# Optimization experiments

Measured on AMD Instinct MI355X. Metric: run time of the kernel, lower is better.

## Reference

```python
import jax, jax.numpy as jnp
import numpy as np


def setup_inputs() -> dict:
    key = jax.random.key(0)
    ks = jax.random.split(key, 7)
    B, NU, NI, F, L = 16384, 100000, 100000, 512, 256
    x = jax.random.randint(ks[0], (B, 2), 0, min(NU, NI), dtype=jnp.int64)
    user_lookup = jax.random.normal(ks[1], (NU, F), dtype=jnp.float32)
    item_lookup = jax.random.normal(ks[2], (NI, F), dtype=jnp.float32)
    s = 1.0 / np.sqrt(F)
    user_W = jax.random.normal(ks[3], (L, F), dtype=jnp.float32) * s
    user_b = jax.random.normal(ks[4], (L,), dtype=jnp.float32) * s
    item_W = jax.random.normal(ks[5], (L, F), dtype=jnp.float32) * s
    item_b = jax.random.normal(ks[6], (L,), dtype=jnp.float32) * s
    return {"x": x, "user_lookup": user_lookup, "item_lookup": item_lookup,
            "user_W": user_W, "user_b": user_b, "item_W": item_W, "item_b": item_b}


def _encode(feats, W, b):
    # Linear (torch weight layout [out, in]) + relu, the mDA encoder
    return jax.nn.relu(jnp.einsum('bf,lf->bl', feats, W) + b)


def reference(x, user_lookup, item_lookup, user_W, user_b, item_W, item_b):
    user_x = user_lookup[x[:, 0]]            # [B, F] gather
    item_x = item_lookup[x[:, 1]]            # [B, F] gather
    user_latent = _encode(user_x, user_W, user_b)   # [B, L]
    item_latent = _encode(item_x, item_W, item_b)   # [B, L]
    # diag(U @ I.T) == rowwise dot; same math, no [B,B] intermediate
    diagonal = jnp.sum(user_latent * item_latent, axis=-1)
    return diagonal[:, None]                 # [B, 1]
```

## Files before the change

### kernel.cpp

```cpp
#include <hip/hip_runtime.h>
#include <stdint.h>

#define B_TOTAL 16384
#define F 512
#define L 256
#define TB 32
#define KC 64
#define LDP 72

typedef _Float16 half8 __attribute__((ext_vector_type(8)));
typedef float floatx4 __attribute__((ext_vector_type(4)));

__device__ __align__(16) _Float16 g_wt[2][8][L][KC];

__global__ void wconv_kernel(const float* __restrict__ uW,
                             const float* __restrict__ iW) {
    int tid = blockIdx.x * blockDim.x + threadIdx.x;
    int which = tid >> 17;
    int r = tid & 131071;
    int l = r >> 9;
    int f = r & 511;
    float v = which ? iW[r] : uW[r];
    g_wt[which][f >> 6][l][f & 63] = (_Float16)v;
}

__launch_bounds__(256, 3)
__global__ void fused_kernel(const int* __restrict__ x,
                             const float* __restrict__ ulook,
                             const float* __restrict__ ilook,
                             const float* __restrict__ ub,
                             const float* __restrict__ ib,
                             float* __restrict__ out) {
    __shared__ _Float16 sA[TB][LDP];
    __shared__ _Float16 sB[L][LDP];
    __shared__ float    sRed[TB];
    __shared__ int      sIdx[2][TB];

    const int t = threadIdx.x;
    const int bbase = blockIdx.x * TB;

    if (t < 2 * TB) {
        int r = t >> 1, c = t & 1;
        sIdx[c][r] = x[(bbase + r) * 2 + c];
    }
    if (t < TB) sRed[t] = 0.0f;
    __syncthreads();

    const int wave = t >> 6;
    const int lane = t & 63;
    const int l15  = lane & 15;
    const int quad = lane >> 4;
    const int nbase = wave * 64;

    floatx4 ulat[2][4];
    floatx4 acc[2][4];

    const int arow = t >> 3;
    const int aoff = (t & 7) * 8;

    #pragma unroll 1
    for (int pass = 0; pass < 2; ++pass) {
        const float* __restrict__ look = pass ? ilook : ulook;
        const float* __restrict__ bias = pass ? ib : ub;

        #pragma unroll
        for (int mt = 0; mt < 2; ++mt)
            #pragma unroll
            for (int nt = 0; nt < 4; ++nt) {
                floatx4 z = {0.f, 0.f, 0.f, 0.f};
                acc[mt][nt] = z;
            }

        const int rowidx = sIdx[pass][arow];
        const float* asrc_base = look + (size_t)rowidx * F + aoff;

        #pragma unroll 1
        for (int ks = 0; ks < 8; ++ks) {
            __syncthreads();

            {
                const float* src = asrc_base + ks * KC;
                float4 v0 = *(const float4*)(src);
                float4 v1 = *(const float4*)(src + 4);
                _Float16 h[8];
                h[0] = (_Float16)v0.x; h[1] = (_Float16)v0.y;
                h[2] = (_Float16)v0.z; h[3] = (_Float16)v0.w;
                h[4] = (_Float16)v1.x; h[5] = (_Float16)v1.y;
                h[6] = (_Float16)v1.z; h[7] = (_Float16)v1.w;
                *(half8*)(&sA[arow][aoff]) = *(half8*)h;
            }
            {
                const _Float16* src = &g_wt[pass][ks][0][0];
                #pragma unroll
                for (int i = 0; i < 8; ++i) {
                    int c = t + 256 * i;
                    int rowb = c >> 3;
                    int offb = (c & 7) * 8;
                    uint4 v = *(const uint4*)(src + c * 8);
                    *(uint4*)(&sB[rowb][offb]) = v;
                }
            }
            __syncthreads();

            #pragma unroll
            for (int kt = 0; kt < 2; ++kt) {
                half8 af[2], bfr[4];
                #pragma unroll
                for (int mt = 0; mt < 2; ++mt)
                    af[mt] = *(const half8*)(&sA[mt * 16 + l15][kt * 32 + quad * 8]);
                #pragma unroll
                for (int nt = 0; nt < 4; ++nt)
                    bfr[nt] = *(const half8*)(&sB[nbase + nt * 16 + l15][kt * 32 + quad * 8]);
                #pragma unroll
                for (int mt = 0; mt < 2; ++mt)
                    #pragma unroll
                    for (int nt = 0; nt < 4; ++nt)
                        acc[mt][nt] = __builtin_amdgcn_mfma_f32_16x16x32_f16(
                            af[mt], bfr[nt], acc[mt][nt], 0, 0, 0);
            }
        }

        if (pass == 0) {
            #pragma unroll
            for (int mt = 0; mt < 2; ++mt)
                #pragma unroll
                for (int nt = 0; nt < 4; ++nt) {
                    int n = nbase + nt * 16 + l15;
                    float bv = bias[n];
                    #pragma unroll
                    for (int r = 0; r < 4; ++r) {
                        float v = acc[mt][nt][r] + bv;
                        ulat[mt][nt][r] = v > 0.f ? v : 0.f;
                    }
                }
        } else {
            #pragma unroll
            for (int mt = 0; mt < 2; ++mt) {
                float partial[4] = {0.f, 0.f, 0.f, 0.f};
                #pragma unroll
                for (int nt = 0; nt < 4; ++nt) {
                    int n = nbase + nt * 16 + l15;
                    float bv = bias[n];
                    #pragma unroll
                    for (int r = 0; r < 4; ++r) {
                        float v = acc[mt][nt][r] + bv;
                        v = v > 0.f ? v : 0.f;
                        partial[r] += v * ulat[mt][nt][r];
                    }
                }
                #pragma unroll
                for (int r = 0; r < 4; ++r) {
                    float v = partial[r];
                    v += __shfl_xor(v, 1);
                    v += __shfl_xor(v, 2);
                    v += __shfl_xor(v, 4);
                    v += __shfl_xor(v, 8);
                    if (l15 == 0)
                        atomicAdd(&sRed[mt * 16 + quad * 4 + r], v);
                }
            }
        }
    }

    __syncthreads();
    if (t < TB) out[bbase + t] = sRed[t];
}

extern "C" void kernel_launch(void* const* d_in, const int* in_sizes, int n_in,
                              void* d_out, int out_size, void* d_ws, size_t ws_size,
                              hipStream_t stream) {
    const int*   x     = (const int*)d_in[0];
    const float* ulook = (const float*)d_in[1];
    const float* ilook = (const float*)d_in[2];
    const float* uW    = (const float*)d_in[3];
    const float* ub    = (const float*)d_in[4];
    const float* iW    = (const float*)d_in[5];
    const float* ib    = (const float*)d_in[6];
    float* out = (float*)d_out;

    wconv_kernel<<<1024, 256, 0, stream>>>(uW, iW);
    fused_kernel<<<B_TOTAL / TB, 256, 0, stream>>>(x, ulook, ilook, ub, ib, out);
}
```

Measured before the change: 346.1 us.

## Load weight fragments directly from global and prefetch gathered rows

The shared-memory staging of the fp16 weight tile is removed, and each wave now reads its MFMA B fragments straight from the global pre-converted weight buffer, relying on L2/L1 caching. The gathered embedding-row load for the next K-chunk is issued before the MFMA work of the current chunk to overlap latency. Launch bounds occupancy hint drops from 3 to 2 blocks per CU, and LDS use shrinks. The risk is that the direct global B reads, each wave fetching 64-row strided fragments, are less efficient than the coalesced LDS staging and add latency on the MFMA critical path.

```diff
diff --git a/kernel.cpp b/kernel.cpp
--- a/kernel.cpp
+++ b/kernel.cpp
@@ -18,13 +18,12 @@
     int tid = blockIdx.x * blockDim.x + threadIdx.x;
     int which = tid >> 17;
     int r = tid & 131071;
-    int l = r >> 9;
     int f = r & 511;
     float v = which ? iW[r] : uW[r];
-    g_wt[which][f >> 6][l][f & 63] = (_Float16)v;
+    g_wt[which][f >> 6][r >> 9][f & 63] = (_Float16)v;
 }
 
-__launch_bounds__(256, 3)
+__launch_bounds__(256, 2)
 __global__ void fused_kernel(const int* __restrict__ x,
                              const float* __restrict__ ulook,
                              const float* __restrict__ ilook,
@@ -32,7 +31,6 @@
                              const float* __restrict__ ib,
                              float* __restrict__ out) {
     __shared__ _Float16 sA[TB][LDP];
-    __shared__ _Float16 sB[L][LDP];
     __shared__ float    sRed[TB];
     __shared__ int      sIdx[2][TB];
 
@@ -72,52 +70,53 @@
             }
 
         const int rowidx = sIdx[pass][arow];
-        const float* asrc_base = look + (size_t)rowidx * F + aoff;
+        const float* asrc = look + (size_t)rowidx * F + aoff;
+
+        float4 p0 = *(const float4*)(asrc);
+        float4 p1 = *(const float4*)(asrc + 4);
 
         #pragma unroll 1
         for (int ks = 0; ks < 8; ++ks) {
             __syncthreads();
 
             {
-                const float* src = asrc_base + ks * KC;
-                float4 v0 = *(const float4*)(src);
-                float4 v1 = *(const float4*)(src + 4);
                 _Float16 h[8];
-                h[0] = (_Float16)v0.x; h[1] = (_Float16)v0.y;
-                h[2] = (_Float16)v0.z; h[3] = (_Float16)v0.w;
-                h[4] = (_Float16)v1.x; h[5] = (_Float16)v1.y;
-                h[6] = (_Float16)v1.z; h[7] = (_Float16)v1.w;
+                h[0] = (_Float16)p0.x; h[1] = (_Float16)p0.y;
+                h[2] = (_Float16)p0.z; h[3] = (_Float16)p0.w;
+                h[4] = (_Float16)p1.x; h[5] = (_Float16)p1.y;
+                h[6] = (_Float16)p1.z; h[7] = (_Float16)p1.w;
                 *(half8*)(&sA[arow][aoff]) = *(half8*)h;
             }
-            {
-                const _Float16* src = &g_wt[pass][ks][0][0];
-                #pragma unroll
-                for (int i = 0; i < 8; ++i) {
-                    int c = t + 256 * i;
-                    int rowb = c >> 3;
-                    int offb = (c & 7) * 8;
-                    uint4 v = *(const uint4*)(src + c * 8);
-                    *(uint4*)(&sB[rowb][offb]) = v;
-                }
+            if (ks < 7) {
+                const float* src = asrc + (ks + 1) * KC;
+                p0 = *(const float4*)(src);
+                p1 = *(const float4*)(src + 4);
             }
             __syncthreads();
 
+            const _Float16* __restrict__ bb = &g_wt[pass][ks][0][0];
+            half8 bfr[2][4];
             #pragma unroll
-            for (int kt = 0; kt < 2; ++kt) {
-                half8 af[2], bfr[4];
+            for (int kt = 0; kt < 2; ++kt)
+                #pragma unroll
+                for (int nt = 0; nt < 4; ++nt)
+                    bfr[kt][nt] = *(const half8*)(bb + (nbase + nt * 16 + l15) * KC
+                                                     + kt * 32 + quad * 8);
+            half8 af[2][2];
+            #pragma unroll
+            for (int kt = 0; kt < 2; ++kt)
                 #pragma unroll
                 for (int mt = 0; mt < 2; ++mt)
-                    af[mt] = *(const half8*)(&sA[mt * 16 + l15][kt * 32 + quad * 8]);
-                #pragma unroll
-                for (int nt = 0; nt < 4; ++nt)
-                    bfr[nt] = *(const half8*)(&sB[nbase + nt * 16 + l15][kt * 32 + quad * 8]);
+                    af[kt][mt] = *(const half8*)(&sA[mt * 16 + l15][kt * 32 + quad * 8]);
+
+            #pragma unroll
+            for (int kt = 0; kt < 2; ++kt)
                 #pragma unroll
                 for (int mt = 0; mt < 2; ++mt)
                     #pragma unroll
                     for (int nt = 0; nt < 4; ++nt)
                         acc[mt][nt] = __builtin_amdgcn_mfma_f32_16x16x32_f16(
-                            af[mt], bfr[nt], acc[mt][nt], 0, 0, 0);
-            }
+                            af[kt][mt], bfr[kt][nt], acc[mt][nt], 0, 0, 0);
         }
 
         if (pass == 0) {
```

New measurement: 359.3 us. 3.8% more time.
